# Optimization experiments

Hardware: AMD Instinct MI355X
Metric: run time of the kernel (lower is better)

## Reference

```python
import jax, jax.numpy as jnp
import numpy as np

B, S, A, D, C = 64, 512, 8, 128, 1024
NUM_CLS = 34


def setup_inputs() -> dict:
    key = jax.random.key(0)
    k1, k2, k3, k4, k5 = jax.random.split(key, 5)
    word_repr = jax.random.normal(k1, (B, S, A, D), dtype=jnp.float32)
    anchor_cls = jax.random.randint(k2, (B, S, A), 0, NUM_CLS, dtype=jnp.int32)
    anchor_loc = jax.random.randint(k3, (B, S, A, 2), 0, 16, dtype=jnp.int32)
    # exactly C candidates per sentence so the view to [B, C, D] is valid
    batch_idx = jnp.repeat(jnp.arange(B, dtype=jnp.int32), C)
    wid = jax.random.randint(k4, (B * C,), 0, S, dtype=jnp.int32)
    aid = jax.random.randint(k5, (B * C,), 0, A, dtype=jnp.int32)
    candidates_idx = jnp.stack([batch_idx, wid, aid], axis=1)  # [B*C, 3]
    return {
        "word_repr": word_repr,
        "anchor_cls": anchor_cls,
        "anchor_loc": anchor_loc,
        "candidates_idx": candidates_idx,
        "batch_candidate_num": C,
    }


def reference(word_repr, anchor_cls, anchor_loc, candidates_idx, batch_candidate_num):
    Bb, Ss, Aa, Dd = word_repr.shape
    Cc = batch_candidate_num
    b, w, a = candidates_idx[:, 0], candidates_idx[:, 1], candidates_idx[:, 2]
    # multi-dim gather: [B*C, D]
    batch_candidates_repr = word_repr[b, w, a, :].reshape(Bb, Cc, Dd)
    batch_candidates_label = anchor_cls[b, w, a].reshape(Bb, Cc)
    candidate_loc = anchor_loc[b, w, a]  # [B*C, 2]
    # invalid candidate: start == end -> mask 0
    candidate_mask = (candidate_loc[:, 0] != candidate_loc[:, 1]).astype(
        word_repr.dtype
    ).reshape(Bb, Cc)
    candidate_len = jnp.sum(candidate_mask, axis=1)
    # nonzero=True: force len >= 1
    candidate_len = jnp.maximum(candidate_len, jnp.asarray(1, candidate_len.dtype))
    candidate_loc = candidate_loc.reshape(Bb, Cc, 2)
    batch_candidates_repr = batch_candidates_repr * candidate_mask[..., None]
    return (
        batch_candidates_repr,
        batch_candidates_label,
        batch_candidate_num,
        candidate_len,
        candidate_mask,
        candidate_loc,
    )
```

## Files before the change

kernel.cpp:

```cpp
#include <hip/hip_runtime.h>

#define BB   64
#define SS   512
#define AA   8
#define DD   128
#define CC   1024
#define NCAND (BB * CC)

#define OFF_REPR  0ULL
#define SZ_REPR   ((size_t)BB * CC * DD)
#define OFF_LABEL (OFF_REPR + SZ_REPR)
#define OFF_NUM   (OFF_LABEL + (size_t)BB * CC)
#define OFF_LEN   (OFF_NUM + 1ULL)
#define OFF_MASK  (OFF_LEN + (size_t)BB)
#define OFF_LOC   (OFF_MASK + (size_t)BB * CC)

__global__ __launch_bounds__(256) void repr_kernel(
    const float* __restrict__ word_repr,
    const int*   __restrict__ anchor_loc,
    const int*   __restrict__ cand_idx,
    float*       __restrict__ out)
{
    const int tid  = threadIdx.x;
    const int lane = tid & 31;
    const int i    = blockIdx.x * 8 + (tid >> 5);

    const int b = cand_idx[3 * i + 0];
    const int w = cand_idx[3 * i + 1];
    const int a = cand_idx[3 * i + 2];
    const int base = (b * SS + w) * AA + a;

    const int l0 = anchor_loc[2 * base + 0];
    const int l1 = anchor_loc[2 * base + 1];
    const float m = (l0 != l1) ? 1.0f : 0.0f;

    const float4 v = ((const float4*)word_repr)[(size_t)base * 32 + lane];
    float4 r;
    r.x = v.x * m; r.y = v.y * m; r.z = v.z * m; r.w = v.w * m;
    ((float4*)(out + OFF_REPR))[(size_t)i * 32 + lane] = r;
}

__global__ __launch_bounds__(256) void scalar_kernel(
    const int* __restrict__ anchor_cls,
    const int* __restrict__ anchor_loc,
    const int* __restrict__ cand_idx,
    const int* __restrict__ cnum,
    float*     __restrict__ out)
{
    const int b   = blockIdx.x;
    const int tid = threadIdx.x;

    float msum = 0.0f;
#pragma unroll
    for (int j = 0; j < CC / 256; ++j) {
        const int c = tid + j * 256;
        const int i = b * CC + c;
        const int bb = cand_idx[3 * i + 0];
        const int w  = cand_idx[3 * i + 1];
        const int a  = cand_idx[3 * i + 2];
        const int base = (bb * SS + w) * AA + a;
        const int l0 = anchor_loc[2 * base + 0];
        const int l1 = anchor_loc[2 * base + 1];
        const float m = (l0 != l1) ? 1.0f : 0.0f;
        msum += m;
        out[OFF_LABEL + i] = (float)anchor_cls[base];
        out[OFF_MASK  + i] = m;
        out[OFF_LOC + 2 * (size_t)i + 0] = (float)l0;
        out[OFF_LOC + 2 * (size_t)i + 1] = (float)l1;
    }

#pragma unroll
    for (int off = 32; off > 0; off >>= 1)
        msum += __shfl_down(msum, off, 64);

    __shared__ float sm[4];
    if ((tid & 63) == 0) sm[tid >> 6] = msum;
    __syncthreads();
    if (tid == 0) {
        const float s = sm[0] + sm[1] + sm[2] + sm[3];
        out[OFF_LEN + b] = fmaxf(s, 1.0f);
        if (b == 0) out[OFF_NUM] = (float)(*cnum);
    }
}

extern "C" void kernel_launch(void* const* d_in, const int* in_sizes, int n_in,
                              void* d_out, int out_size, void* d_ws, size_t ws_size,
                              hipStream_t stream) {
    const float* word_repr  = (const float*)d_in[0];
    const int*   anchor_cls = (const int*)  d_in[1];
    const int*   anchor_loc = (const int*)  d_in[2];
    const int*   cand_idx   = (const int*)  d_in[3];
    const int*   cnum       = (const int*)  d_in[4];
    float*       out        = (float*)      d_out;

    repr_kernel<<<dim3(NCAND / 8), dim3(256), 0, stream>>>(
        word_repr, anchor_loc, cand_idx, out);
    scalar_kernel<<<dim3(BB), dim3(256), 0, stream>>>(
        anchor_cls, anchor_loc, cand_idx, cnum, out);
}
```

Measured before the change: 195.8 us.

## Fuse scalar outputs and mask-length reduction into the gather kernel

Merges the two kernels into one launch. Each 32-lane group writes the label, mask and location scalars from lane 0, and the first BB blocks also recompute the per-batch mask count for candidate_len. The anchor_loc pair is now read as a single int2. This removes one kernel launch and the serialized second pass, at the cost of making the first 64 blocks do extra gather work that re-reads indices and locations.

```diff
diff --git a/kernel.cpp b/kernel.cpp
--- a/kernel.cpp
+++ b/kernel.cpp
@@ -15,10 +15,12 @@
 #define OFF_MASK  (OFF_LEN + (size_t)BB)
 #define OFF_LOC   (OFF_MASK + (size_t)BB * CC)
 
-__global__ __launch_bounds__(256) void repr_kernel(
+__global__ __launch_bounds__(256) void fused_kernel(
     const float* __restrict__ word_repr,
+    const int*   __restrict__ anchor_cls,
     const int*   __restrict__ anchor_loc,
     const int*   __restrict__ cand_idx,
+    const int*   __restrict__ cnum,
     float*       __restrict__ out)
 {
     const int tid  = threadIdx.x;
@@ -30,56 +32,46 @@
     const int a = cand_idx[3 * i + 2];
     const int base = (b * SS + w) * AA + a;
 
-    const int l0 = anchor_loc[2 * base + 0];
-    const int l1 = anchor_loc[2 * base + 1];
-    const float m = (l0 != l1) ? 1.0f : 0.0f;
+    const int2 loc = ((const int2*)anchor_loc)[base];
+    const float m = (loc.x != loc.y) ? 1.0f : 0.0f;
 
     const float4 v = ((const float4*)word_repr)[(size_t)base * 32 + lane];
     float4 r;
     r.x = v.x * m; r.y = v.y * m; r.z = v.z * m; r.w = v.w * m;
     ((float4*)(out + OFF_REPR))[(size_t)i * 32 + lane] = r;
-}
 
-__global__ __launch_bounds__(256) void scalar_kernel(
-    const int* __restrict__ anchor_cls,
-    const int* __restrict__ anchor_loc,
-    const int* __restrict__ cand_idx,
-    const int* __restrict__ cnum,
-    float*     __restrict__ out)
-{
-    const int b   = blockIdx.x;
-    const int tid = threadIdx.x;
-
-    float msum = 0.0f;
-#pragma unroll
-    for (int j = 0; j < CC / 256; ++j) {
-        const int c = tid + j * 256;
-        const int i = b * CC + c;
-        const int bb = cand_idx[3 * i + 0];
-        const int w  = cand_idx[3 * i + 1];
-        const int a  = cand_idx[3 * i + 2];
-        const int base = (bb * SS + w) * AA + a;
-        const int l0 = anchor_loc[2 * base + 0];
-        const int l1 = anchor_loc[2 * base + 1];
-        const float m = (l0 != l1) ? 1.0f : 0.0f;
-        msum += m;
+    if (lane == 0) {
         out[OFF_LABEL + i] = (float)anchor_cls[base];
         out[OFF_MASK  + i] = m;
-        out[OFF_LOC + 2 * (size_t)i + 0] = (float)l0;
-        out[OFF_LOC + 2 * (size_t)i + 1] = (float)l1;
+        out[OFF_LOC + 2 * (size_t)i + 0] = (float)loc.x;
+        out[OFF_LOC + 2 * (size_t)i + 1] = (float)loc.y;
     }
 
+    if (blockIdx.x < BB) {
+        const int bb = blockIdx.x;
+        float msum = 0.0f;
 #pragma unroll
-    for (int off = 32; off > 0; off >>= 1)
-        msum += __shfl_down(msum, off, 64);
+        for (int j = 0; j < CC / 256; ++j) {
+            const int c  = tid + j * 256;
+            const int i2 = bb * CC + c;
+            const int b2 = cand_idx[3 * i2 + 0];
+            const int w2 = cand_idx[3 * i2 + 1];
+            const int a2 = cand_idx[3 * i2 + 2];
+            const int2 l2 = ((const int2*)anchor_loc)[(b2 * SS + w2) * AA + a2];
+            msum += (l2.x != l2.y) ? 1.0f : 0.0f;
+        }
+#pragma unroll
+        for (int off = 32; off > 0; off >>= 1)
+            msum += __shfl_down(msum, off, 64);
 
-    __shared__ float sm[4];
-    if ((tid & 63) == 0) sm[tid >> 6] = msum;
-    __syncthreads();
-    if (tid == 0) {
-        const float s = sm[0] + sm[1] + sm[2] + sm[3];
-        out[OFF_LEN + b] = fmaxf(s, 1.0f);
-        if (b == 0) out[OFF_NUM] = (float)(*cnum);
+        __shared__ float sm[4];
+        if ((tid & 63) == 0) sm[tid >> 6] = msum;
+        __syncthreads();
+        if (tid == 0) {
+            const float s = sm[0] + sm[1] + sm[2] + sm[3];
+            out[OFF_LEN + bb] = fmaxf(s, 1.0f);
+            if (bb == 0) out[OFF_NUM] = (float)(*cnum);
+        }
     }
 }
 
@@ -93,8 +85,6 @@
     const int*   cnum       = (const int*)  d_in[4];
     float*       out        = (float*)      d_out;
 
-    repr_kernel<<<dim3(NCAND / 8), dim3(256), 0, stream>>>(
-        word_repr, anchor_loc, cand_idx, out);
-    scalar_kernel<<<dim3(BB), dim3(256), 0, stream>>>(
-        anchor_cls, anchor_loc, cand_idx, cnum, out);
+    fused_kernel<<<dim3(NCAND / 8), dim3(256), 0, stream>>>(
+        word_repr, anchor_cls, anchor_loc, cand_idx, cnum, out);
 }
```

Measured after the change: 193.3 us. About the same (-1.3%).
